# Performance work log

Hardware: AMD Instinct MI355X
Metric: run time of the kernel (lower is better)

Reference implementation:

```python
import jax, jax.numpy as jnp
import numpy as np
from jax import lax


def _conv1x1(x, w, b=None):
    # x: [B,C,H,W], w: [O,C]
    y = jnp.einsum('bchw,oc->bohw', x, w)
    if b is not None:
        y = y + b[None, :, None, None]
    return y


def _lgce(x, pre_w, pre_b, w1, b1, w2, b2, sw, sb, post_w, post_b):
    # Local Group Context Enhancer on [B,64,H,W], 8 groups of 8 channels.
    b, c, h, wd = x.shape
    g = 8
    cg = c // g
    res = x
    x = _conv1x1(x, pre_w, pre_b)
    xg = x.reshape(b, g, cg, h, wd)
    # CBAM per group (vectorized over groups)
    pooled = xg.mean(axis=(3, 4))                                  # [b,g,cg]
    hid = jax.nn.relu(jnp.einsum('bgc,ghc->bgh', pooled, w1) + b1[None])
    cw = jax.nn.sigmoid(jnp.einsum('bgh,gch->bgc', hid, w2) + b2[None])
    xc = xg * cw[:, :, :, None, None]                              # channel gate
    sp = jax.nn.sigmoid(jnp.einsum('bgchw,goc->bgohw', xc, sw) + sb[None, :, :, None, None])
    cbam_out = xc * sp                                             # spatial gate
    resp = jax.nn.sigmoid(cbam_out)
    thr = resp.mean(axis=(2, 3, 4), keepdims=True)                 # per (batch, group)
    mask = jnp.where(resp > thr, jnp.ones_like(resp), resp)
    x = (xg * mask).reshape(b, c, h, wd)
    x = _conv1x1(x, post_w, post_b)
    return x + res


def setup_inputs() -> dict:
    key = jax.random.key(0)
    ks = jax.random.split(key, 20)
    f = lambda k, s: (jax.random.normal(k, s) * 0.02).astype(jnp.float32)
    return {
        'x': jax.random.normal(ks[0], (4, 128, 256, 256), dtype=jnp.float32),
        'input_proj_w': f(ks[1], (128, 128)),
        'lgce_pre_w': f(ks[2], (64, 64)), 'lgce_pre_b': f(ks[3], (64,)),
        'cbam_w1': f(ks[4], (8, 2, 8)), 'cbam_b1': f(ks[5], (8, 2)),
        'cbam_w2': f(ks[6], (8, 8, 2)), 'cbam_b2': f(ks[7], (8, 8)),
        'cbam_sw': f(ks[8], (8, 1, 8)), 'cbam_sb': f(ks[9], (8, 1)),
        'lgce_post_w': f(ks[10], (64, 64)), 'lgce_post_b': f(ks[11], (64,)),
        'qkv_w': f(ks[12], (192, 64)),
        'dw_w': f(ks[13], (192, 1, 3, 3)),
        'gate_w1': f(ks[14], (32, 64)), 'gate_b1': f(ks[15], (32,)),
        'gate_w2': f(ks[16], (1, 32)), 'gate_b2': f(ks[17], (1,)),
        'temperature': jnp.ones((8, 1, 1), jnp.float32),
        'scales': jnp.full((4,), 0.2, jnp.float32),
        'proj_out_w': f(ks[18], (128, 128)),
    }


def reference(x, input_proj_w, lgce_pre_w, lgce_pre_b, cbam_w1, cbam_b1,
              cbam_w2, cbam_b2, cbam_sw, cbam_sb, lgce_post_w, lgce_post_b,
              qkv_w, dw_w, gate_w1, gate_b1, gate_w2, gate_b2,
              temperature, scales, proj_out_w):
    b, c, h, wd = x.shape
    heads = 8
    proj = _conv1x1(x, input_proj_w)
    lb, gb = jnp.split(proj, 2, axis=1)                            # local / global
    lb = _lgce(lb, lgce_pre_w, lgce_pre_b, cbam_w1, cbam_b1, cbam_w2, cbam_b2,
               cbam_sw, cbam_sb, lgce_post_w, lgce_post_b)
    qkv = _conv1x1(gb, qkv_w)
    qkv = lax.conv_general_dilated(qkv, dw_w, (1, 1), 'SAME',
                                   feature_group_count=192,
                                   dimension_numbers=('NCHW', 'OIHW', 'NCHW'))
    q, k, v = jnp.split(qkv, 3, axis=1)
    hw = h * wd
    cph = (c // 2) // heads                                        # channels per head
    to_heads = lambda t: t.reshape(b, heads, cph, hw)
    q, k, v = to_heads(q), to_heads(k), to_heads(v)
    q = q / jnp.maximum(jnp.linalg.norm(q, axis=-1, keepdims=True), 1e-12)
    k = k / jnp.maximum(jnp.linalg.norm(k, axis=-1, keepdims=True), 1e-12)
    attn = jnp.einsum('bhcn,bhdn->bhcd', q, k) * temperature[None]  # [b,h,cph,cph]
    # dynamic top-k from global gate (single scalar over whole batch, as original)
    gate = jax.nn.sigmoid(_conv1x1(jax.nn.relu(_conv1x1(gb, gate_w1, gate_b1)),
                                   gate_w2, gate_b2))
    kdyn = jnp.clip(jnp.floor(cph * gate.mean()), 1.0, float(cph))
    # rank-based top-k mask (jit-safe equivalent of topk+scatter)
    ranks = jnp.argsort(jnp.argsort(-attn, axis=-1), axis=-1)
    attn = jnp.where(ranks < kdyn, attn, -jnp.inf)
    attn = jax.nn.softmax(attn, axis=-1)
    out = jnp.einsum('bhcd,bhdn->bhcn', attn, v) * scales.sum()
    out = out.reshape(b, c // 2, h, wd)
    fused = jnp.concatenate([out, lb], axis=1)
    return _conv1x1(fused, proj_out_w)
```

## Files before the change

kernel.cpp:

```cpp
#include <hip/hip_runtime.h>
#include <math.h>

#define HWN 65536

typedef __attribute__((ext_vector_type(8))) short bf16x8;
typedef __attribute__((ext_vector_type(4))) float f32x4;

__device__ __forceinline__ float sgm(float x){ return 1.0f/(1.0f+expf(-x)); }

__device__ __forceinline__ unsigned pack_hi2(float a, float b){
    return (__float_as_uint(b) & 0xFFFF0000u) | (__float_as_uint(a) >> 16);
}

__device__ __forceinline__ void fma4(float acc[4], const float4 w,
                                     const float4 x0, const float4 x1,
                                     const float4 x2, const float4 x3){
    acc[0] += w.x*x0.x + w.y*x1.x + w.z*x2.x + w.w*x3.x;
    acc[1] += w.x*x0.y + w.y*x1.y + w.z*x2.y + w.w*x3.y;
    acc[2] += w.x*x0.z + w.y*x1.z + w.z*x2.z + w.w*x3.z;
    acc[3] += w.x*x0.w + w.y*x1.w + w.z*x2.w + w.w*x3.w;
}

__global__ __launch_bounds__(256,2) void k1_proj(
    const float* __restrict__ x,   const float* __restrict__ Wp,
    const float* __restrict__ Wpre,const float* __restrict__ bpre,
    const float* __restrict__ Wqkv,
    const float* __restrict__ Wg1, const float* __restrict__ bg1,
    const float* __restrict__ wg2, const float* __restrict__ bg2,
    float* __restrict__ lb, float* __restrict__ pre, float* __restrict__ qkv,
    float* __restrict__ pooled_part, float* __restrict__ gate_part)
{
    __shared__ float st[128*128];
    float4* st4 = (float4*)st;
    float*  ht  = st;

    const int t    = threadIdx.x;
    const int blk  = blockIdx.x;
    const int b    = blk >> 9;
    const int p0   = (blk & 511) << 7;
    const int pg   = t & 15;
    const int og   = t >> 4;
    const int slot = blk & 63;

    const float4* x4 = (const float4*)x;

    #pragma unroll
    for (int i = 0; i < 16; ++i) {
        int idx = t + 256*i;
        int c = idx >> 5, q = idx & 31;
        st4[c*32 + q] = x4[(size_t)(b*128 + c)*16384 + (p0>>2) + q];
    }
    __syncthreads();

    {
        const int o0 = og*8;
        float acc[8][8];
        #pragma unroll
        for (int j=0;j<8;++j)
            #pragma unroll
            for (int k=0;k<8;++k) acc[j][k]=0.f;
        const float4* W4 = (const float4*)Wp;
        #pragma unroll 2
        for (int c = 0; c < 128; c += 4) {
            float4 xa0 = st4[(c+0)*32 + pg],      xb0 = st4[(c+0)*32 + 16 + pg];
            float4 xa1 = st4[(c+1)*32 + pg],      xb1 = st4[(c+1)*32 + 16 + pg];
            float4 xa2 = st4[(c+2)*32 + pg],      xb2 = st4[(c+2)*32 + 16 + pg];
            float4 xa3 = st4[(c+3)*32 + pg],      xb3 = st4[(c+3)*32 + 16 + pg];
            #pragma unroll
            for (int j = 0; j < 8; ++j) {
                float4 w = W4[(o0+j)*32 + (c>>2)];
                fma4(&acc[j][0], w, xa0,xa1,xa2,xa3);
                fma4(&acc[j][4], w, xb0,xb1,xb2,xb3);
            }
        }
        __syncthreads();

        #pragma unroll
        for (int j = 0; j < 8; ++j) {
            st4[(o0+j)*32 + pg]      = make_float4(acc[j][0],acc[j][1],acc[j][2],acc[j][3]);
            st4[(o0+j)*32 + 16 + pg] = make_float4(acc[j][4],acc[j][5],acc[j][6],acc[j][7]);
        }
        if (og < 8) {
            float4* lb4 = (float4*)lb;
            #pragma unroll
            for (int j = 0; j < 8; ++j) {
                lb4[(size_t)(b*64 + o0+j)*16384 + (p0>>2) + pg] =
                    make_float4(acc[j][0],acc[j][1],acc[j][2],acc[j][3]);
                lb4[(size_t)(b*64 + o0+j)*16384 + (p0>>2) + 16 + pg] =
                    make_float4(acc[j][4],acc[j][5],acc[j][6],acc[j][7]);
            }
        }
    }
    __syncthreads();

    {
        const int o0 = og*4;
        float acc[4][8];
        #pragma unroll
        for (int j=0;j<4;++j)
            #pragma unroll
            for (int k=0;k<8;++k) acc[j][k]=0.f;
        const float4* W4 = (const float4*)Wpre;
        #pragma unroll 2
        for (int c = 0; c < 64; c += 4) {
            float4 xa0 = st4[(c+0)*32 + pg],      xb0 = st4[(c+0)*32 + 16 + pg];
            float4 xa1 = st4[(c+1)*32 + pg],      xb1 = st4[(c+1)*32 + 16 + pg];
            float4 xa2 = st4[(c+2)*32 + pg],      xb2 = st4[(c+2)*32 + 16 + pg];
            float4 xa3 = st4[(c+3)*32 + pg],      xb3 = st4[(c+3)*32 + 16 + pg];
            #pragma unroll
            for (int j = 0; j < 4; ++j) {
                float4 w = W4[(o0+j)*16 + (c>>2)];
                fma4(&acc[j][0], w, xa0,xa1,xa2,xa3);
                fma4(&acc[j][4], w, xb0,xb1,xb2,xb3);
            }
        }
        float4* pre4 = (float4*)pre;
        #pragma unroll
        for (int j = 0; j < 4; ++j) {
            float bs = bpre[o0+j];
            float4 v0 = make_float4(acc[j][0]+bs, acc[j][1]+bs, acc[j][2]+bs, acc[j][3]+bs);
            float4 v1 = make_float4(acc[j][4]+bs, acc[j][5]+bs, acc[j][6]+bs, acc[j][7]+bs);
            pre4[(size_t)(b*64 + o0+j)*16384 + (p0>>2) + pg]      = v0;
            pre4[(size_t)(b*64 + o0+j)*16384 + (p0>>2) + 16 + pg] = v1;
            float s = v0.x+v0.y+v0.z+v0.w + v1.x+v1.y+v1.z+v1.w;
            s += __shfl_xor(s,1); s += __shfl_xor(s,2);
            s += __shfl_xor(s,4); s += __shfl_xor(s,8);
            if (pg == 0) atomicAdd(&pooled_part[slot*256 + b*64 + o0 + j], s);
        }
    }

    #pragma unroll
    for (int chk = 0; chk < 2; ++chk) {
        const int o0 = og*12 + chk*6;
        float acc[6][8];
        #pragma unroll
        for (int j=0;j<6;++j)
            #pragma unroll
            for (int k=0;k<8;++k) acc[j][k]=0.f;
        const float4* W4 = (const float4*)Wqkv;
        #pragma unroll 2
        for (int c = 0; c < 64; c += 4) {
            float4 xa0 = st4[(64+c+0)*32 + pg],   xb0 = st4[(64+c+0)*32 + 16 + pg];
            float4 xa1 = st4[(64+c+1)*32 + pg],   xb1 = st4[(64+c+1)*32 + 16 + pg];
            float4 xa2 = st4[(64+c+2)*32 + pg],   xb2 = st4[(64+c+2)*32 + 16 + pg];
            float4 xa3 = st4[(64+c+3)*32 + pg],   xb3 = st4[(64+c+3)*32 + 16 + pg];
            #pragma unroll
            for (int j = 0; j < 6; ++j) {
                float4 w = W4[(o0+j)*16 + (c>>2)];
                fma4(&acc[j][0], w, xa0,xa1,xa2,xa3);
                fma4(&acc[j][4], w, xb0,xb1,xb2,xb3);
            }
        }
        float4* qkv4 = (float4*)qkv;
        #pragma unroll
        for (int j = 0; j < 6; ++j) {
            qkv4[(size_t)(b*192 + o0+j)*16384 + (p0>>2) + pg] =
                make_float4(acc[j][0],acc[j][1],acc[j][2],acc[j][3]);
            qkv4[(size_t)(b*192 + o0+j)*16384 + (p0>>2) + 16 + pg] =
                make_float4(acc[j][4],acc[j][5],acc[j][6],acc[j][7]);
        }
    }

    {
        const int o0 = og*2;
        float acc[2][8];
        #pragma unroll
        for (int j=0;j<2;++j)
            #pragma unroll
            for (int k=0;k<8;++k) acc[j][k]=0.f;
        const float4* W4 = (const float4*)Wg1;
        for (int c = 0; c < 64; c += 4) {
            float4 xa0 = st4[(64+c+0)*32 + pg],   xb0 = st4[(64+c+0)*32 + 16 + pg];
            float4 xa1 = st4[(64+c+1)*32 + pg],   xb1 = st4[(64+c+1)*32 + 16 + pg];
            float4 xa2 = st4[(64+c+2)*32 + pg],   xb2 = st4[(64+c+2)*32 + 16 + pg];
            float4 xa3 = st4[(64+c+3)*32 + pg],   xb3 = st4[(64+c+3)*32 + 16 + pg];
            #pragma unroll
            for (int j = 0; j < 2; ++j) {
                float4 w = W4[(o0+j)*16 + (c>>2)];
                fma4(&acc[j][0], w, xa0,xa1,xa2,xa3);
                fma4(&acc[j][4], w, xb0,xb1,xb2,xb3);
            }
        }
        __syncthreads();
        #pragma unroll
        for (int j = 0; j < 2; ++j) {
            float bs = bg1[o0+j];
            #pragma unroll
            for (int k = 0; k < 4; ++k) {
                ht[(o0+j)*128 + pg*4 + k]      = fmaxf(acc[j][k]+bs,   0.0f);
                ht[(o0+j)*128 + 64 + pg*4 + k] = fmaxf(acc[j][4+k]+bs, 0.0f);
            }
        }
    }
    __syncthreads();

    if (t < 128) {
        float g = bg2[0];
        #pragma unroll
        for (int c = 0; c < 32; ++c) g += wg2[c]*ht[c*128 + t];
        g = sgm(g);
        g += __shfl_xor(g,1);  g += __shfl_xor(g,2);  g += __shfl_xor(g,4);
        g += __shfl_xor(g,8);  g += __shfl_xor(g,16); g += __shfl_xor(g,32);
        if ((t & 63) == 0) atomicAdd(&gate_part[slot], g);
    }
}

__global__ void k2_small(const float* __restrict__ pooled_part,
                         const float* __restrict__ gate_part,
                         const float* __restrict__ w1, const float* __restrict__ b1,
                         const float* __restrict__ w2, const float* __restrict__ b2,
                         float* __restrict__ cw, float* __restrict__ kdyn)
{
    __shared__ float pl[256];
    const int t = threadIdx.x;
    float s = 0.f;
    for (int sl = 0; sl < 64; ++sl) s += pooled_part[sl*256 + t];
    pl[t] = s * (1.0f/65536.0f);
    __syncthreads();
    const int b = t >> 6, g = (t >> 3) & 7, c = t & 7;
    float h0 = b1[g*2+0], h1 = b1[g*2+1];
    #pragma unroll
    for (int cc = 0; cc < 8; ++cc) {
        float p = pl[b*64 + g*8 + cc];
        h0 += p*w1[g*16 + 0*8 + cc];
        h1 += p*w1[g*16 + 1*8 + cc];
    }
    h0 = fmaxf(h0, 0.f); h1 = fmaxf(h1, 0.f);
    cw[t] = sgm(h0*w2[g*16 + c*2 + 0] + h1*w2[g*16 + c*2 + 1] + b2[g*8+c]);
    if (t == 0) {
        float gs = 0.f;
        for (int sl = 0; sl < 64; ++sl) gs += gate_part[sl];
        float kd = floorf(8.0f * (gs * (1.0f/262144.0f)));
        *kdyn = fminf(fmaxf(kd, 1.0f), 8.0f);
    }
}

#define K4_ROWSTRIDE 264
#define K4_BUF (10*K4_ROWSTRIDE)

__global__ __launch_bounds__(256,3) void k4_dw(
    const float* __restrict__ qkv, const float* __restrict__ dww,
    const float* __restrict__ pre, const float* __restrict__ cw,
    const float* __restrict__ sw,  const float* __restrict__ sb,
    float* __restrict__ v, float* __restrict__ Sg, float* __restrict__ sumsq,
    float* __restrict__ thr_sum)
{
    __shared__ float sh[2*K4_BUF];

    const int t    = threadIdx.x;
    const int b    = blockIdx.x >> 8;
    const int h    = (blockIdx.x >> 5) & 7;
    const int band = blockIdx.x & 31;
    const int r0   = band * 8;
    const int lr   = t >> 5;
    const int c0   = (t & 31) * 4;
    const int lane = t & 63;

    if (t < 40) {
        int bufi = t / 20, r = (t % 20) >> 1, side = t & 1;
        sh[bufi*K4_BUF + r*K4_ROWSTRIDE + (side ? 260 : 3)] = 0.0f;
    }

    float4 reg[3];

    auto issue_loads = [&](int ch) {
        const float4* base = (const float4*)(qkv + (size_t)(b*192 + ch)*HWN);
        #pragma unroll
        for (int j = 0; j < 3; ++j) {
            int i = t + 256*j;
            float4 val = make_float4(0.f,0.f,0.f,0.f);
            if (i < 640) {
                int row = i >> 6, col4 = i & 63;
                int gy = r0 - 1 + row;
                if (gy >= 0 && gy < 256) val = base[gy*64 + col4];
            }
            reg[j] = val;
        }
    };

    auto write_lds = [&](float* buf) {
        #pragma unroll
        for (int j = 0; j < 3; ++j) {
            int i = t + 256*j;
            if (i < 640) {
                int row = i >> 6, col4 = i & 63;
                *(float4*)&buf[row*K4_ROWSTRIDE + 4 + col4*4] = reg[j];
            }
        }
    };

    auto conv8 = [&](const float* buf, const float* __restrict__ w9, float out[8]) {
        #pragma unroll
        for (int g = 0; g < 2; ++g) {
            const int cc = c0 + g*128;
            float a0=0.f, a1=0.f, a2=0.f, a3=0.f;
            #pragma unroll
            for (int rr = 0; rr < 3; ++rr) {
                const float* row = &buf[(lr+rr)*K4_ROWSTRIDE + 4 + cc];
                float4 m = *(const float4*)row;
                float l = row[-1], r = row[4];
                float w0 = w9[rr*3+0], w1 = w9[rr*3+1], w2 = w9[rr*3+2];
                a0 = fmaf(w0,l,   fmaf(w1,m.x, fmaf(w2,m.y, a0)));
                a1 = fmaf(w0,m.x, fmaf(w1,m.y, fmaf(w2,m.z, a1)));
                a2 = fmaf(w0,m.y, fmaf(w1,m.z, fmaf(w2,m.w, a2)));
                a3 = fmaf(w0,m.z, fmaf(w1,m.w, fmaf(w2,r,   a3)));
            }
            out[g*4+0]=a0; out[g*4+1]=a1; out[g*4+2]=a2; out[g*4+3]=a3;
        }
    };

    auto wsum = [&](float val) {
        val += __shfl_xor(val,1);  val += __shfl_xor(val,2);  val += __shfl_xor(val,4);
        val += __shfl_xor(val,8);  val += __shfl_xor(val,16); val += __shfl_xor(val,32);
        return val;
    };

    float dq[8][8];

    float* sq_q = &sumsq[b*128 + h*8];
    float* sq_k = &sumsq[b*128 + 64 + h*8];
    float* Sgb  = &Sg[(size_t)(b*8+h)*64];

    issue_loads(h*8 + 0);

    #pragma unroll
    for (int ch = 0; ch < 8; ++ch) {
        float* buf = sh + (ch & 1)*K4_BUF;
        write_lds(buf);
        issue_loads(ch < 7 ? (h*8 + ch + 1) : (64 + h*8));
        __syncthreads();
        conv8(buf, dww + (h*8 + ch)*9, dq[ch]);
        float ss = 0.f;
        #pragma unroll
        for (int p = 0; p < 8; ++p) ss = fmaf(dq[ch][p], dq[ch][p], ss);
        ss = wsum(ss);
        if (lane == 0) atomicAdd(&sq_q[ch], ss);
    }

    #pragma unroll
    for (int ch = 0; ch < 8; ++ch) {
        float* buf = sh + (ch & 1)*K4_BUF;
        write_lds(buf);
        issue_loads(ch < 7 ? (64 + h*8 + ch + 1) : (128 + h*8));
        __syncthreads();
        float dk[8];
        conv8(buf, dww + (64 + h*8 + ch)*9, dk);
        float ss = 0.f;
        #pragma unroll
        for (int p = 0; p < 8; ++p) ss = fmaf(dk[p], dk[p], ss);
        ss = wsum(ss);
        if (lane == 0) atomicAdd(&sq_k[ch], ss);
        #pragma unroll
        for (int c = 0; c < 8; ++c) {
            float acc = 0.f;
            #pragma unroll
            for (int p = 0; p < 8; ++p) acc = fmaf(dq[c][p], dk[p], acc);
            acc = wsum(acc);
            if (lane == 0) atomicAdd(&Sgb[c*8 + ch], acc);
        }
    }

    #pragma unroll
    for (int ch = 0; ch < 8; ++ch) {
        float* buf = sh + (ch & 1)*K4_BUF;
        write_lds(buf);
        if (ch < 7) issue_loads(128 + h*8 + ch + 1);
        __syncthreads();
        float dv[8];
        conv8(buf, dww + (128 + h*8 + ch)*9, dv);
        float* vb = v + (size_t)(b*64 + h*8 + ch)*HWN + (r0 + lr)*256;
        *(float4*)&vb[c0]       = make_float4(dv[0],dv[1],dv[2],dv[3]);
        *(float4*)&vb[c0 + 128] = make_float4(dv[4],dv[5],dv[6],dv[7]);
    }

    {
        float cwr[8], swr[8];
        #pragma unroll
        for (int c = 0; c < 8; ++c) {
            cwr[c] = cw[b*64 + h*8 + c];
            swr[c] = sw[h*8 + c];
        }
        const float sbg = sb[h];
        float rs = 0.f;
        const float* preb = pre + (size_t)(b*64 + h*8)*HWN + (size_t)(r0 + lr)*256;
        #pragma unroll
        for (int g2 = 0; g2 < 2; ++g2) {
            const int cc = c0 + g2*128;
            float xc[8][4];
            float spa0 = sbg, spa1 = sbg, spa2 = sbg, spa3 = sbg;
            #pragma unroll
            for (int c = 0; c < 8; ++c) {
                float4 xv = *(const float4*)&preb[(size_t)c*HWN + cc];
                xc[c][0] = xv.x*cwr[c]; xc[c][1] = xv.y*cwr[c];
                xc[c][2] = xv.z*cwr[c]; xc[c][3] = xv.w*cwr[c];
                spa0 = fmaf(xc[c][0], swr[c], spa0);
                spa1 = fmaf(xc[c][1], swr[c], spa1);
                spa2 = fmaf(xc[c][2], swr[c], spa2);
                spa3 = fmaf(xc[c][3], swr[c], spa3);
            }
            float sp0 = sgm(spa0), sp1 = sgm(spa1), sp2 = sgm(spa2), sp3 = sgm(spa3);
            #pragma unroll
            for (int c = 0; c < 8; ++c) {
                rs += sgm(xc[c][0]*sp0);
                rs += sgm(xc[c][1]*sp1);
                rs += sgm(xc[c][2]*sp2);
                rs += sgm(xc[c][3]*sp3);
            }
        }
        rs = wsum(rs);
        if (lane == 0) atomicAdd(&thr_sum[b*8 + h], rs);
    }
}

__global__ void k6_attn(const float* __restrict__ Sg, const float* __restrict__ sumsq,
                        const float* __restrict__ temp, const float* __restrict__ kdynp,
                        const float* __restrict__ thr_sum, const float* __restrict__ scales,
                        float* __restrict__ A, float* __restrict__ thr)
{
    const int t = threadIdx.x;
    if (t < 32) thr[t] = thr_sum[t] * (1.0f/(8.0f*65536.0f));
    const int b = t >> 6, h = (t >> 3) & 7, c = t & 7;
    const float kd = *kdynp;
    const float ssum = scales[0]+scales[1]+scales[2]+scales[3];
    const float nq = fmaxf(sqrtf(sumsq[b*128 + h*8 + c]), 1e-12f);
    const float tv = temp[h];
    const float* Srow = Sg + (size_t)(b*8+h)*64 + c*8;
    float a[8];
    #pragma unroll
    for (int d = 0; d < 8; ++d) {
        float nk = fmaxf(sqrtf(sumsq[b*128 + 64 + h*8 + d]), 1e-12f);
        a[d] = Srow[d] / (nq*nk) * tv;
    }
    bool keep[8];
    #pragma unroll
    for (int d = 0; d < 8; ++d) {
        int r = 0;
        #pragma unroll
        for (int e = 0; e < 8; ++e)
            r += (a[e] > a[d]) || (a[e] == a[d] && e < d);
        keep[d] = ((float)r < kd);
    }
    float m = -INFINITY;
    #pragma unroll
    for (int d = 0; d < 8; ++d) if (keep[d]) m = fmaxf(m, a[d]);
    float ex[8]; float sum = 0.f;
    #pragma unroll
    for (int d = 0; d < 8; ++d) { ex[d] = keep[d] ? expf(a[d]-m) : 0.f; sum += ex[d]; }
    const float inv = ssum / sum;
    #pragma unroll
    for (int d = 0; d < 8; ++d)
        A[(size_t)(b*8+h)*64 + c*8 + d] = ex[d]*inv;
}

__global__ __launch_bounds__(256,2) void k7_final(
    const float* __restrict__ pre, const float* __restrict__ lb, const float* __restrict__ v,
    const float* __restrict__ cw,  const float* __restrict__ thr,
    const float* __restrict__ sw,  const float* __restrict__ sb,
    const float* __restrict__ A,
    const float* __restrict__ Wpost, const float* __restrict__ bpost,
    const float* __restrict__ Wout,  float* __restrict__ out)
{
    __shared__ float smem[16384];
    float* pr = smem;
    float* vt = smem + 8192;
    float4* pr4 = (float4*)pr;
    float4* vt4 = (float4*)vt;
    unsigned* XPhi32 = (unsigned*)smem;
    unsigned* XPlo32 = (unsigned*)(smem + 4096);
    const unsigned short* XPhi = (const unsigned short*)smem;
    const unsigned short* XPlo = (const unsigned short*)(smem + 4096);
    unsigned* XThi32 = (unsigned*)smem;
    unsigned* XTlo32 = (unsigned*)(smem + 8192);
    const unsigned short* XThi = (const unsigned short*)smem;
    const unsigned short* XTlo = (const unsigned short*)(smem + 8192);

    const int t   = threadIdx.x;
    const int blk = blockIdx.x;
    const int b   = blk >> 9;
    const int p0  = (blk & 511) << 7;
    const int pg  = t & 15;
    const int og  = t >> 4;
    const int lane = t & 63, wv = t >> 6;
    const int lm = lane & 15, lq = lane >> 4;

    const float4* pre4g = (const float4*)pre;
    const float4* v4g   = (const float4*)v;
    #pragma unroll
    for (int i = 0; i < 8; ++i) {
        int idx = t + 256*i;
        int c = idx >> 5, q = idx & 31;
        size_t gi = (size_t)(b*64 + c)*16384 + (p0>>2) + q;
        pr4[c*32+q] = pre4g[gi];
        vt4[c*32+q] = v4g[gi];
    }
    __syncthreads();

    float mk[4][8];
    #pragma unroll
    for (int s = 0; s < 4; ++s) {
        int task = t + 256*s;
        int g = task >> 7, px = task & 127;
        float xc[8], xv[8];
        float spa = sb[g];
        #pragma unroll
        for (int c = 0; c < 8; ++c) {
            xv[c] = pr[(g*8+c)*128 + px];
            xc[c] = xv[c]*cw[b*64 + g*8 + c];
            spa += xc[c]*sw[g*8 + c];
        }
        float sp = sgm(spa);
        float th = thr[b*8 + g];
        #pragma unroll
        for (int c = 0; c < 8; ++c) {
            float resp = sgm(xc[c]*sp);
            float mask = resp > th ? 1.0f : resp;
            mk[s][c] = xv[c]*mask;
        }
    }
    __syncthreads();

    #pragma unroll
    for (int s = 0; s < 4; ++s) {
        int task = t + 256*s;
        int g = task >> 7, px = task & 127;
        const int sw2 = (px & 7) << 2;
        const int rowb = px*32;
        #pragma unroll
        for (int c = 0; c < 8; c += 2) {
            float e0 = mk[s][c], e1 = mk[s][c+1];
            int i32 = (rowb + g*4 + (c>>1)) ^ sw2;
            XPhi32[i32] = pack_hi2(e0, e1);
            float h0 = __uint_as_float(__float_as_uint(e0)&0xFFFF0000u);
            float h1 = __uint_as_float(__float_as_uint(e1)&0xFFFF0000u);
            XPlo32[i32] = pack_hi2(e0-h0, e1-h1);
        }
    }
    __syncthreads();

    float postv[8][4];
    {
        const int ot = wv;
        const int orow = ot*16 + lm;
        f32x4 acc[8];
        #pragma unroll
        for (int pt = 0; pt < 8; ++pt) { acc[pt][0]=0.f; acc[pt][1]=0.f; acc[pt][2]=0.f; acc[pt][3]=0.f; }
        #pragma unroll
        for (int kk = 0; kk < 2; ++kk) {
            const int cbase = kk*32 + lq*8;
            const float* wp = Wpost + orow*64 + cbase;
            float4 w0 = *(const float4*)wp;
            float4 w1 = *(const float4*)(wp+4);
            float we[8] = {w0.x,w0.y,w0.z,w0.w,w1.x,w1.y,w1.z,w1.w};
            bf16x8 Ahi, Alo;
            #pragma unroll
            for (int d = 0; d < 4; ++d) {
                float e0 = we[2*d], e1 = we[2*d+1];
                ((unsigned*)&Ahi)[d] = pack_hi2(e0, e1);
                float h0 = __uint_as_float(__float_as_uint(e0)&0xFFFF0000u);
                float h1 = __uint_as_float(__float_as_uint(e1)&0xFFFF0000u);
                ((unsigned*)&Alo)[d] = pack_hi2(e0-h0, e1-h1);
            }
            #pragma unroll
            for (int pt = 0; pt < 8; ++pt) {
                const int px = pt*16 + lm;
                const int idx = (px*64 + cbase) ^ ((px&7)<<3);
                bf16x8 Bhi = *(const bf16x8*)&XPhi[idx];
                bf16x8 Blo = *(const bf16x8*)&XPlo[idx];
                acc[pt] = __builtin_amdgcn_mfma_f32_16x16x32_bf16(Ahi, Bhi, acc[pt], 0,0,0);
                acc[pt] = __builtin_amdgcn_mfma_f32_16x16x32_bf16(Ahi, Blo, acc[pt], 0,0,0);
                acc[pt] = __builtin_amdgcn_mfma_f32_16x16x32_bf16(Alo, Bhi, acc[pt], 0,0,0);
            }
        }
        #pragma unroll
        for (int pt = 0; pt < 8; ++pt) {
            const int px = p0 + pt*16 + lm;
            #pragma unroll
            for (int r = 0; r < 4; ++r) {
                const int ch = ot*16 + lq*4 + r;
                postv[pt][r] = acc[pt][r] + bpost[ch]
                             + lb[(size_t)(b*64 + ch)*HWN + px];
            }
        }
    }

    float attv[4][8];
    {
        const int ch0 = og*4;
        #pragma unroll
        for (int j = 0; j < 4; ++j) {
            int ch = ch0 + j;
            int hh = ch >> 3, c = ch & 7;
            const float* Ar = A + (size_t)(b*8+hh)*64 + c*8;
            float a0=0.f,a1=0.f,a2=0.f,a3=0.f,a4=0.f,a5=0.f,a6=0.f,a7=0.f;
            #pragma unroll
            for (int d = 0; d < 8; ++d) {
                float av = Ar[d];
                float4 v0 = vt4[(hh*8+d)*32 + pg];
                float4 v1 = vt4[(hh*8+d)*32 + 16 + pg];
                a0 += av*v0.x; a1 += av*v0.y; a2 += av*v0.z; a3 += av*v0.w;
                a4 += av*v1.x; a5 += av*v1.y; a6 += av*v1.z; a7 += av*v1.w;
            }
            attv[j][0]=a0; attv[j][1]=a1; attv[j][2]=a2; attv[j][3]=a3;
            attv[j][4]=a4; attv[j][5]=a5; attv[j][6]=a6; attv[j][7]=a7;
        }
    }
    __syncthreads();

    {
        #pragma unroll
        for (int half = 0; half < 2; ++half) {
            #pragma unroll
            for (int k = 0; k < 4; ++k) {
                const int px = half*64 + pg*4 + k;
                const int sw2 = (px & 7) << 2;
                const int rowb = px*64;
                #pragma unroll
                for (int jj = 0; jj < 4; jj += 2) {
                    float a0 = attv[jj][half*4+k], a1 = attv[jj+1][half*4+k];
                    int i32 = (rowb + ((og*4+jj)>>1)) ^ sw2;
                    XThi32[i32] = pack_hi2(a0, a1);
                    float ah0 = __uint_as_float(__float_as_uint(a0)&0xFFFF0000u);
                    float ah1 = __uint_as_float(__float_as_uint(a1)&0xFFFF0000u);
                    XTlo32[i32] = pack_hi2(a0-ah0, a1-ah1);
                }
            }
        }
    }
    {
        const int ot = wv;
        const int colb = 32 + ((ot*16 + lq*4) >> 1);
        #pragma unroll
        for (int pt = 0; pt < 8; ++pt) {
            const int px = pt*16 + lm;
            const int sw2 = (px & 7) << 2;
            const int rowb = px*64;
            float q0 = postv[pt][0], q1 = postv[pt][1];
            int i32 = (rowb + colb) ^ sw2;
            XThi32[i32] = pack_hi2(q0, q1);
            float h0 = __uint_as_float(__float_as_uint(q0)&0xFFFF0000u);
            float h1 = __uint_as_float(__float_as_uint(q1)&0xFFFF0000u);
            XTlo32[i32] = pack_hi2(q0-h0, q1-h1);
            float q2 = postv[pt][2], q3 = postv[pt][3];
            i32 = (rowb + colb + 1) ^ sw2;
            XThi32[i32] = pack_hi2(q2, q3);
            float h2 = __uint_as_float(__float_as_uint(q2)&0xFFFF0000u);
            float h3 = __uint_as_float(__float_as_uint(q3)&0xFFFF0000u);
            XTlo32[i32] = pack_hi2(q2-h2, q3-h3);
        }
    }
    __syncthreads();

    {
        #pragma unroll
        for (int oo = 0; oo < 2; ++oo) {
            const int ot = wv*2 + oo;
            f32x4 acc[8];
            #pragma unroll
            for (int pt = 0; pt < 8; ++pt) { acc[pt][0]=0.f; acc[pt][1]=0.f; acc[pt][2]=0.f; acc[pt][3]=0.f; }
            const int orow = ot*16 + lm;
            #pragma unroll
            for (int kk = 0; kk < 4; ++kk) {
                const int cbase = kk*32 + lq*8;
                const float* wp = Wout + orow*128 + cbase;
                float4 w0 = *(const float4*)wp;
                float4 w1 = *(const float4*)(wp+4);
                float we[8] = {w0.x,w0.y,w0.z,w0.w,w1.x,w1.y,w1.z,w1.w};
                bf16x8 Ahi, Alo;
                #pragma unroll
                for (int d = 0; d < 4; ++d) {
                    float e0 = we[2*d], e1 = we[2*d+1];
                    ((unsigned*)&Ahi)[d] = pack_hi2(e0, e1);
                    float h0 = __uint_as_float(__float_as_uint(e0)&0xFFFF0000u);
                    float h1 = __uint_as_float(__float_as_uint(e1)&0xFFFF0000u);
                    ((unsigned*)&Alo)[d] = pack_hi2(e0-h0, e1-h1);
                }
                #pragma unroll
                for (int pt = 0; pt < 8; ++pt) {
                    const int px = pt*16 + lm;
                    const int idx = (px*128 + cbase) ^ ((px&7)<<3);
                    bf16x8 Bhi = *(const bf16x8*)&XThi[idx];
                    bf16x8 Blo = *(const bf16x8*)&XTlo[idx];
                    acc[pt] = __builtin_amdgcn_mfma_f32_16x16x32_bf16(Ahi, Bhi, acc[pt], 0,0,0);
                    acc[pt] = __builtin_amdgcn_mfma_f32_16x16x32_bf16(Ahi, Blo, acc[pt], 0,0,0);
                    acc[pt] = __builtin_amdgcn_mfma_f32_16x16x32_bf16(Alo, Bhi, acc[pt], 0,0,0);
                }
            }
            #pragma unroll
            for (int pt = 0; pt < 8; ++pt) {
                const int px = p0 + pt*16 + lm;
                #pragma unroll
                for (int r = 0; r < 4; ++r) {
                    const int ch = ot*16 + lq*4 + r;
                    out[(size_t)(b*128 + ch)*HWN + px] = acc[pt][r];
                }
            }
        }
    }
}

extern "C" void kernel_launch(void* const* d_in, const int* in_sizes, int n_in,
                              void* d_out, int out_size, void* d_ws, size_t ws_size,
                              hipStream_t stream)
{
    const float* x     = (const float*)d_in[0];
    const float* Wp    = (const float*)d_in[1];
    const float* Wpre  = (const float*)d_in[2];
    const float* bpre  = (const float*)d_in[3];
    const float* w1    = (const float*)d_in[4];
    const float* b1    = (const float*)d_in[5];
    const float* w2    = (const float*)d_in[6];
    const float* b2    = (const float*)d_in[7];
    const float* sw    = (const float*)d_in[8];
    const float* sb    = (const float*)d_in[9];
    const float* Wpost = (const float*)d_in[10];
    const float* bpost = (const float*)d_in[11];
    const float* Wqkv  = (const float*)d_in[12];
    const float* dww   = (const float*)d_in[13];
    const float* Wg1   = (const float*)d_in[14];
    const float* bg1   = (const float*)d_in[15];
    const float* wg2   = (const float*)d_in[16];
    const float* bg2   = (const float*)d_in[17];
    const float* temp  = (const float*)d_in[18];
    const float* scales= (const float*)d_in[19];
    const float* Wout  = (const float*)d_in[20];
    float* out = (float*)d_out;

    float* ws = (float*)d_ws;
    float* pooled_part = ws;
    float* gate_part   = ws + 16384;
    float* thr_sum     = ws + 16448;
    float* sumsq       = ws + 16480;
    float* Sg          = ws + 16992;
    float* cw          = ws + 19040;
    float* kdyn        = ws + 19296;
    float* thr         = ws + 19328;
    float* A           = ws + 19360;

    float* lb  = ws + 32768;
    float* pre = lb  + 16777216;
    float* qkv = pre + 16777216;
    float* v   = qkv + 50331648;

    hipMemsetAsync(ws, 0, (size_t)19040*sizeof(float), stream);

    k1_proj <<<2048, 256, 0, stream>>>(x, Wp, Wpre, bpre, Wqkv, Wg1, bg1, wg2, bg2,
                                       lb, pre, qkv, pooled_part, gate_part);
    k2_small<<<1,    256, 0, stream>>>(pooled_part, gate_part, w1, b1, w2, b2, cw, kdyn);
    k4_dw   <<<1024, 256, 0, stream>>>(qkv, dww, pre, cw, sw, sb, v, Sg, sumsq, thr_sum);
    k6_attn <<<1,    256, 0, stream>>>(Sg, sumsq, temp, kdyn, thr_sum, scales, A, thr);
    k7_final<<<2048, 256, 0, stream>>>(pre, lb, v, cw, thr, sw, sb, A,
                                       Wpost, bpost, Wout, out);
}
```

Before: 714.6 us.

## Halve k7 shared memory by splitting output GEMM K-dimension into two passes

The final kernel no longer stages v in shared memory; the attention-times-v product reads v directly from global memory. The 128-wide output projection is split into two K=64 passes (post-LGCE half, then attention half) that accumulate into persistent registers and reuse one 32 KB bf16 hi/lo buffer. This cuts LDS from 64 KB to 32 KB per block, which can allow more resident blocks, at the cost of holding 16 accumulator tiles across passes (more register pressure) and one extra barrier.

```diff
diff --git a/kernel.cpp b/kernel.cpp
--- a/kernel.cpp
+++ b/kernel.cpp
@@ -460,19 +460,13 @@
     const float* __restrict__ Wpost, const float* __restrict__ bpost,
     const float* __restrict__ Wout,  float* __restrict__ out)
 {
-    __shared__ float smem[16384];
+    __shared__ float smem[8192];
     float* pr = smem;
-    float* vt = smem + 8192;
     float4* pr4 = (float4*)pr;
-    float4* vt4 = (float4*)vt;
-    unsigned* XPhi32 = (unsigned*)smem;
-    unsigned* XPlo32 = (unsigned*)(smem + 4096);
-    const unsigned short* XPhi = (const unsigned short*)smem;
-    const unsigned short* XPlo = (const unsigned short*)(smem + 4096);
-    unsigned* XThi32 = (unsigned*)smem;
-    unsigned* XTlo32 = (unsigned*)(smem + 8192);
-    const unsigned short* XThi = (const unsigned short*)smem;
-    const unsigned short* XTlo = (const unsigned short*)(smem + 8192);
+    unsigned* Bhi32 = (unsigned*)smem;
+    unsigned* Blo32 = (unsigned*)(smem + 4096);
+    const unsigned short* Bhi16 = (const unsigned short*)smem;
+    const unsigned short* Blo16 = (const unsigned short*)(smem + 4096);
 
     const int t   = threadIdx.x;
     const int blk = blockIdx.x;
@@ -484,14 +478,11 @@
     const int lm = lane & 15, lq = lane >> 4;
 
     const float4* pre4g = (const float4*)pre;
-    const float4* v4g   = (const float4*)v;
     #pragma unroll
     for (int i = 0; i < 8; ++i) {
         int idx = t + 256*i;
         int c = idx >> 5, q = idx & 31;
-        size_t gi = (size_t)(b*64 + c)*16384 + (p0>>2) + q;
-        pr4[c*32+q] = pre4g[gi];
-        vt4[c*32+q] = v4g[gi];
+        pr4[c*32+q] = pre4g[(size_t)(b*64 + c)*16384 + (p0>>2) + q];
     }
     __syncthreads();
 
@@ -529,10 +520,10 @@
         for (int c = 0; c < 8; c += 2) {
             float e0 = mk[s][c], e1 = mk[s][c+1];
             int i32 = (rowb + g*4 + (c>>1)) ^ sw2;
-            XPhi32[i32] = pack_hi2(e0, e1);
+            Bhi32[i32] = pack_hi2(e0, e1);
             float h0 = __uint_as_float(__float_as_uint(e0)&0xFFFF0000u);
             float h1 = __uint_as_float(__float_as_uint(e1)&0xFFFF0000u);
-            XPlo32[i32] = pack_hi2(e0-h0, e1-h1);
+            Blo32[i32] = pack_hi2(e0-h0, e1-h1);
         }
     }
     __syncthreads();
@@ -564,11 +555,11 @@
             for (int pt = 0; pt < 8; ++pt) {
                 const int px = pt*16 + lm;
                 const int idx = (px*64 + cbase) ^ ((px&7)<<3);
-                bf16x8 Bhi = *(const bf16x8*)&XPhi[idx];
-                bf16x8 Blo = *(const bf16x8*)&XPlo[idx];
-                acc[pt] = __builtin_amdgcn_mfma_f32_16x16x32_bf16(Ahi, Bhi, acc[pt], 0,0,0);
-                acc[pt] = __builtin_amdgcn_mfma_f32_16x16x32_bf16(Ahi, Blo, acc[pt], 0,0,0);
-                acc[pt] = __builtin_amdgcn_mfma_f32_16x16x32_bf16(Alo, Bhi, acc[pt], 0,0,0);
+                bf16x8 Bh = *(const bf16x8*)&Bhi16[idx];
+                bf16x8 Bl = *(const bf16x8*)&Blo16[idx];
+                acc[pt] = __builtin_amdgcn_mfma_f32_16x16x32_bf16(Ahi, Bh, acc[pt], 0,0,0);
+                acc[pt] = __builtin_amdgcn_mfma_f32_16x16x32_bf16(Ahi, Bl, acc[pt], 0,0,0);
+                acc[pt] = __builtin_amdgcn_mfma_f32_16x16x32_bf16(Alo, Bh, acc[pt], 0,0,0);
             }
         }
         #pragma unroll
@@ -585,23 +576,89 @@
 
     float attv[4][8];
     {
-        const int ch0 = og*4;
-        #pragma unroll
-        for (int j = 0; j < 4; ++j) {
-            int ch = ch0 + j;
-            int hh = ch >> 3, c = ch & 7;
-            const float* Ar = A + (size_t)(b*8+hh)*64 + c*8;
-            float a0=0.f,a1=0.f,a2=0.f,a3=0.f,a4=0.f,a5=0.f,a6=0.f,a7=0.f;
-            #pragma unroll
-            for (int d = 0; d < 8; ++d) {
-                float av = Ar[d];
-                float4 v0 = vt4[(hh*8+d)*32 + pg];
-                float4 v1 = vt4[(hh*8+d)*32 + 16 + pg];
-                a0 += av*v0.x; a1 += av*v0.y; a2 += av*v0.z; a3 += av*v0.w;
-                a4 += av*v1.x; a5 += av*v1.y; a6 += av*v1.z; a7 += av*v1.w;
-            }
-            attv[j][0]=a0; attv[j][1]=a1; attv[j][2]=a2; attv[j][3]=a3;
-            attv[j][4]=a4; attv[j][5]=a5; attv[j][6]=a6; attv[j][7]=a7;
+        const int hh = og >> 1;
+        const int cb = (og & 1) * 4;
+        const float* Ab = A + (size_t)(b*8+hh)*64;
+        #pragma unroll
+        for (int j = 0; j < 4; ++j)
+            #pragma unroll
+            for (int k = 0; k < 8; ++k) attv[j][k] = 0.f;
+        const float* vb = v + (size_t)(b*64 + hh*8)*HWN + p0;
+        #pragma unroll
+        for (int d = 0; d < 8; ++d) {
+            float4 v0 = *(const float4*)&vb[(size_t)d*HWN + pg*4];
+            float4 v1 = *(const float4*)&vb[(size_t)d*HWN + 64 + pg*4];
+            #pragma unroll
+            for (int j = 0; j < 4; ++j) {
+                float av = Ab[(cb+j)*8 + d];
+                attv[j][0] += av*v0.x; attv[j][1] += av*v0.y;
+                attv[j][2] += av*v0.z; attv[j][3] += av*v0.w;
+                attv[j][4] += av*v1.x; attv[j][5] += av*v1.y;
+                attv[j][6] += av*v1.z; attv[j][7] += av*v1.w;
+            }
+        }
+    }
+    __syncthreads();
+
+    {
+        const int ot = wv;
+        const int colb = (ot*16 + lq*4) >> 1;
+        #pragma unroll
+        for (int pt = 0; pt < 8; ++pt) {
+            const int px = pt*16 + lm;
+            const int sw2 = (px & 7) << 2;
+            const int rowb = px*32;
+            float q0 = postv[pt][0], q1 = postv[pt][1];
+            int i32 = (rowb + colb) ^ sw2;
+            Bhi32[i32] = pack_hi2(q0, q1);
+            float h0 = __uint_as_float(__float_as_uint(q0)&0xFFFF0000u);
+            float h1 = __uint_as_float(__float_as_uint(q1)&0xFFFF0000u);
+            Blo32[i32] = pack_hi2(q0-h0, q1-h1);
+            float q2 = postv[pt][2], q3 = postv[pt][3];
+            i32 = (rowb + colb + 1) ^ sw2;
+            Bhi32[i32] = pack_hi2(q2, q3);
+            float h2 = __uint_as_float(__float_as_uint(q2)&0xFFFF0000u);
+            float h3 = __uint_as_float(__float_as_uint(q3)&0xFFFF0000u);
+            Blo32[i32] = pack_hi2(q2-h2, q3-h3);
+        }
+    }
+    __syncthreads();
+
+    f32x4 acc[2][8];
+    #pragma unroll
+    for (int oo = 0; oo < 2; ++oo)
+        #pragma unroll
+        for (int pt = 0; pt < 8; ++pt) { acc[oo][pt][0]=0.f; acc[oo][pt][1]=0.f; acc[oo][pt][2]=0.f; acc[oo][pt][3]=0.f; }
+    #pragma unroll
+    for (int oo = 0; oo < 2; ++oo) {
+        const int ot = wv*2 + oo;
+        const int orow = ot*16 + lm;
+        #pragma unroll
+        for (int kk = 0; kk < 2; ++kk) {
+            const int cl = kk*32 + lq*8;
+            const float* wp = Wout + orow*128 + 64 + cl;
+            float4 w0 = *(const float4*)wp;
+            float4 w1 = *(const float4*)(wp+4);
+            float we[8] = {w0.x,w0.y,w0.z,w0.w,w1.x,w1.y,w1.z,w1.w};
+            bf16x8 Ahi, Alo;
+            #pragma unroll
+            for (int d = 0; d < 4; ++d) {
+                float e0 = we[2*d], e1 = we[2*d+1];
+                ((unsigned*)&Ahi)[d] = pack_hi2(e0, e1);
+                float h0 = __uint_as_float(__float_as_uint(e0)&0xFFFF0000u);
+                float h1 = __uint_as_float(__float_as_uint(e1)&0xFFFF0000u);
+                ((unsigned*)&Alo)[d] = pack_hi2(e0-h0, e1-h1);
+            }
+            #pragma unroll
+            for (int pt = 0; pt < 8; ++pt) {
+                const int px = pt*16 + lm;
+                const int idx = (px*64 + cl) ^ ((px&7)<<3);
+                bf16x8 Bh = *(const bf16x8*)&Bhi16[idx];
+                bf16x8 Bl = *(const bf16x8*)&Blo16[idx];
+                acc[oo][pt] = __builtin_amdgcn_mfma_f32_16x16x32_bf16(Ahi, Bh, acc[oo][pt], 0,0,0);
+                acc[oo][pt] = __builtin_amdgcn_mfma_f32_16x16x32_bf16(Ahi, Bl, acc[oo][pt], 0,0,0);
+                acc[oo][pt] = __builtin_amdgcn_mfma_f32_16x16x32_bf16(Alo, Bh, acc[oo][pt], 0,0,0);
+            }
         }
     }
     __syncthreads();
@@ -613,86 +670,59 @@
             for (int k = 0; k < 4; ++k) {
                 const int px = half*64 + pg*4 + k;
                 const int sw2 = (px & 7) << 2;
-                const int rowb = px*64;
+                const int rowb = px*32;
                 #pragma unroll
                 for (int jj = 0; jj < 4; jj += 2) {
                     float a0 = attv[jj][half*4+k], a1 = attv[jj+1][half*4+k];
                     int i32 = (rowb + ((og*4+jj)>>1)) ^ sw2;
-                    XThi32[i32] = pack_hi2(a0, a1);
+                    Bhi32[i32] = pack_hi2(a0, a1);
                     float ah0 = __uint_as_float(__float_as_uint(a0)&0xFFFF0000u);
                     float ah1 = __uint_as_float(__float_as_uint(a1)&0xFFFF0000u);
-                    XTlo32[i32] = pack_hi2(a0-ah0, a1-ah1);
+                    Blo32[i32] = pack_hi2(a0-ah0, a1-ah1);
                 }
             }
         }
     }
-    {
-        const int ot = wv;
-        const int colb = 32 + ((ot*16 + lq*4) >> 1);
+    __syncthreads();
+
+    #pragma unroll
+    for (int oo = 0; oo < 2; ++oo) {
+        const int ot = wv*2 + oo;
+        const int orow = ot*16 + lm;
+        #pragma unroll
+        for (int kk = 0; kk < 2; ++kk) {
+            const int cl = kk*32 + lq*8;
+            const float* wp = Wout + orow*128 + cl;
+            float4 w0 = *(const float4*)wp;
+            float4 w1 = *(const float4*)(wp+4);
+            float we[8] = {w0.x,w0.y,w0.z,w0.w,w1.x,w1.y,w1.z,w1.w};
+            bf16x8 Ahi, Alo;
+            #pragma unroll
+            for (int d = 0; d < 4; ++d) {
+                float e0 = we[2*d], e1 = we[2*d+1];
+                ((unsigned*)&Ahi)[d] = pack_hi2(e0, e1);
+                float h0 = __uint_as_float(__float_as_uint(e0)&0xFFFF0000u);
+                float h1 = __uint_as_float(__float_as_uint(e1)&0xFFFF0000u);
+                ((unsigned*)&Alo)[d] = pack_hi2(e0-h0, e1-h1);
+            }
+            #pragma unroll
+            for (int pt = 0; pt < 8; ++pt) {
+                const int px = pt*16 + lm;
+                const int idx = (px*64 + cl) ^ ((px&7)<<3);
+                bf16x8 Bh = *(const bf16x8*)&Bhi16[idx];
+                bf16x8 Bl = *(const bf16x8*)&Blo16[idx];
+                acc[oo][pt] = __builtin_amdgcn_mfma_f32_16x16x32_bf16(Ahi, Bh, acc[oo][pt], 0,0,0);
+                acc[oo][pt] = __builtin_amdgcn_mfma_f32_16x16x32_bf16(Ahi, Bl, acc[oo][pt], 0,0,0);
+                acc[oo][pt] = __builtin_amdgcn_mfma_f32_16x16x32_bf16(Alo, Bh, acc[oo][pt], 0,0,0);
+            }
+        }
         #pragma unroll
         for (int pt = 0; pt < 8; ++pt) {
-            const int px = pt*16 + lm;
-            const int sw2 = (px & 7) << 2;
-            const int rowb = px*64;
-            float q0 = postv[pt][0], q1 = postv[pt][1];
-            int i32 = (rowb + colb) ^ sw2;
-            XThi32[i32] = pack_hi2(q0, q1);
-            float h0 = __uint_as_float(__float_as_uint(q0)&0xFFFF0000u);
-            float h1 = __uint_as_float(__float_as_uint(q1)&0xFFFF0000u);
-            XTlo32[i32] = pack_hi2(q0-h0, q1-h1);
-            float q2 = postv[pt][2], q3 = postv[pt][3];
-            i32 = (rowb + colb + 1) ^ sw2;
-            XThi32[i32] = pack_hi2(q2, q3);
-            float h2 = __uint_as_float(__float_as_uint(q2)&0xFFFF0000u);
-            float h3 = __uint_as_float(__float_as_uint(q3)&0xFFFF0000u);
-            XTlo32[i32] = pack_hi2(q2-h2, q3-h3);
-        }
-    }
-    __syncthreads();
-
-    {
-        #pragma unroll
-        for (int oo = 0; oo < 2; ++oo) {
-            const int ot = wv*2 + oo;
-            f32x4 acc[8];
-            #pragma unroll
-            for (int pt = 0; pt < 8; ++pt) { acc[pt][0]=0.f; acc[pt][1]=0.f; acc[pt][2]=0.f; acc[pt][3]=0.f; }
-            const int orow = ot*16 + lm;
-            #pragma unroll
-            for (int kk = 0; kk < 4; ++kk) {
-                const int cbase = kk*32 + lq*8;
-                const float* wp = Wout + orow*128 + cbase;
-                float4 w0 = *(const float4*)wp;
-                float4 w1 = *(const float4*)(wp+4);
-                float we[8] = {w0.x,w0.y,w0.z,w0.w,w1.x,w1.y,w1.z,w1.w};
-                bf16x8 Ahi, Alo;
-                #pragma unroll
-                for (int d = 0; d < 4; ++d) {
-                    float e0 = we[2*d], e1 = we[2*d+1];
-                    ((unsigned*)&Ahi)[d] = pack_hi2(e0, e1);
-                    float h0 = __uint_as_float(__float_as_uint(e0)&0xFFFF0000u);
-                    float h1 = __uint_as_float(__float_as_uint(e1)&0xFFFF0000u);
-                    ((unsigned*)&Alo)[d] = pack_hi2(e0-h0, e1-h1);
-                }
-                #pragma unroll
-                for (int pt = 0; pt < 8; ++pt) {
-                    const int px = pt*16 + lm;
-                    const int idx = (px*128 + cbase) ^ ((px&7)<<3);
-                    bf16x8 Bhi = *(const bf16x8*)&XThi[idx];
-                    bf16x8 Blo = *(const bf16x8*)&XTlo[idx];
-                    acc[pt] = __builtin_amdgcn_mfma_f32_16x16x32_bf16(Ahi, Bhi, acc[pt], 0,0,0);
-                    acc[pt] = __builtin_amdgcn_mfma_f32_16x16x32_bf16(Ahi, Blo, acc[pt], 0,0,0);
-                    acc[pt] = __builtin_amdgcn_mfma_f32_16x16x32_bf16(Alo, Bhi, acc[pt], 0,0,0);
-                }
-            }
-            #pragma unroll
-            for (int pt = 0; pt < 8; ++pt) {
-                const int px = p0 + pt*16 + lm;
-                #pragma unroll
-                for (int r = 0; r < 4; ++r) {
-                    const int ch = ot*16 + lq*4 + r;
-                    out[(size_t)(b*128 + ch)*HWN + px] = acc[pt][r];
-                }
+            const int px = p0 + pt*16 + lm;
+            #pragma unroll
+            for (int r = 0; r < 4; ++r) {
+                const int ch = ot*16 + lq*4 + r;
+                out[(size_t)(b*128 + ch)*HWN + px] = acc[oo][pt][r];
             }
         }
     }
```

New measurement: 765.9 us. 7.2% more time.
